# Kernel tuning notes

Measured on AMD Instinct MI355X. Metric: run time of the kernel, lower is better.

Reference implementation:

```python
import jax, jax.numpy as jnp
import numpy as np

N, E = 50000, 800000
IN_DIM, HID, H1, H2, NCLS = 512, 64, 4, 1, 40
NEG_SLOPE = 0.2


def gat_conv(x, src, dst, W, att_src, att_dst, b, heads, ch):
    # x: [N, F_in]; W: [F_in, heads*ch]; att_*: [heads, ch]; b: [heads*ch]
    n = x.shape[0]
    h = (x @ W).reshape(n, heads, ch)                      # [N,H,C]
    a_s = jnp.einsum('nhc,hc->nh', h, att_src)             # [N,H]
    a_d = jnp.einsum('nhc,hc->nh', h, att_dst)             # [N,H]
    e = jax.nn.leaky_relu(a_s[src] + a_d[dst], NEG_SLOPE)  # [E,H]
    # segment softmax over incoming edges of each destination node
    m = jax.ops.segment_max(e, dst, num_segments=n)        # [N,H]
    ex = jnp.exp(e - m[dst])
    s = jax.ops.segment_sum(ex, dst, num_segments=n)       # [N,H]
    alpha = ex / (s[dst] + 1e-16)                          # [E,H]
    out = jax.ops.segment_sum(alpha[:, :, None] * h[src], dst, num_segments=n)
    return out.reshape(n, heads * ch) + b


def setup_inputs() -> dict:
    key = jax.random.key(0)
    ks = jax.random.split(key, 10)
    glorot = lambda k, shp: jax.random.normal(k, shp, jnp.float32) * jnp.sqrt(2.0 / (shp[0] + shp[-1]))
    return {
        'x': jax.random.normal(ks[0], (N, IN_DIM), jnp.float32),
        'edge_index': jax.random.randint(ks[1], (2, E), 0, N, jnp.int64),
        'W1': glorot(ks[2], (IN_DIM, H1 * HID)),
        'att_src1': glorot(ks[3], (H1, HID)),
        'att_dst1': glorot(ks[4], (H1, HID)),
        'b1': jnp.zeros((H1 * HID,), jnp.float32),
        'W2': glorot(ks[5], (H1 * HID, H2 * NCLS)),
        'att_src2': glorot(ks[6], (H2, NCLS)),
        'att_dst2': glorot(ks[7], (H2, NCLS)),
        'b2': jnp.zeros((H2 * NCLS,), jnp.float32),
    }


def reference(x, edge_index, W1, att_src1, att_dst1, b1, W2, att_src2, att_dst2, b2):
    n = x.shape[0]
    loops = jnp.arange(n, dtype=edge_index.dtype)
    src = jnp.concatenate([edge_index[0], loops])  # add self loops (PyG default)
    dst = jnp.concatenate([edge_index[1], loops])
    # dropout layers are identity in eval mode
    h = gat_conv(x, src, dst, W1, att_src1, att_dst1, b1, H1, HID)
    h = jax.nn.elu(h)
    out = gat_conv(h, src, dst, W2, att_src2, att_dst2, b2, H2, NCLS)
    return jax.nn.log_softmax(out, axis=1)
```

## Files before the change

kernel.cpp:

```cpp
#include <hip/hip_runtime.h>
#include <math.h>
#include <stdint.h>


typedef short bf16x8 __attribute__((ext_vector_type(8)));
typedef float f32x4  __attribute__((ext_vector_type(4)));

static __device__ __forceinline__ float leaky(float x){ return x > 0.f ? x : 0.2f*x; }
static __device__ __forceinline__ unsigned short f2bf(float f){
  uint32_t u = __float_as_uint(f);
  uint32_t r = u + 0x7fffu + ((u >> 16) & 1u);
  return (unsigned short)(r >> 16);
}
static __device__ __forceinline__ float bf2f(unsigned short u){
  return __uint_as_float(((uint32_t)u) << 16);
}

__global__ void k_cvt_x(const float* __restrict__ x, unsigned short* __restrict__ xb, int n4){
  int i = blockIdx.x*blockDim.x + threadIdx.x;
  if (i >= n4) return;
  float4 v = ((const float4*)x)[i];
  ushort4 o; o.x=f2bf(v.x); o.y=f2bf(v.y); o.z=f2bf(v.z); o.w=f2bf(v.w);
  ((ushort4*)xb)[i] = o;
}

__global__ void k_cvt_w(const float* __restrict__ W, unsigned short* __restrict__ wt){
  int i = blockIdx.x*blockDim.x + threadIdx.x;
  if (i >= 512*256) return;
  int k = i >> 8, n = i & 255;
  wt[n*512 + k] = f2bf(W[i]);
}

__global__ void k_count(const int* __restrict__ ei, int E, int n, int* __restrict__ deg){
  int i = blockIdx.x*blockDim.x + threadIdx.x;
  int tot = E + n;
  if (i >= tot) return;
  int dst = (i < E) ? ei[E + i] : (i - E);
  atomicAdd(&deg[dst], 1);
}

__global__ __launch_bounds__(256) void k_scan_a(const int* __restrict__ deg,
    int* __restrict__ rowstart, int* __restrict__ bsum, int n){
  __shared__ int sm[256];
  int b = blockIdx.x, t = threadIdx.x;
  int i = b*256 + t;
  int v = (i < n) ? deg[i] : 0;
  sm[t] = v;
  __syncthreads();
  for (int off=1; off<256; off<<=1){
    int u = (t >= off) ? sm[t-off] : 0;
    __syncthreads();
    sm[t] += u;
    __syncthreads();
  }
  if (i < n) rowstart[i+1] = sm[t];
  if (t == 255) bsum[b] = sm[255];
}
__global__ __launch_bounds__(256) void k_scan_b(int* __restrict__ bsum, int nb){
  __shared__ int sm[256];
  int t = threadIdx.x;
  int v = (t < nb) ? bsum[t] : 0;
  sm[t] = v;
  __syncthreads();
  for (int off=1; off<256; off<<=1){
    int u = (t >= off) ? sm[t-off] : 0;
    __syncthreads();
    sm[t] += u;
    __syncthreads();
  }
  if (t < nb) bsum[t] = sm[t] - v;
}
__global__ __launch_bounds__(256) void k_scan_c(int* __restrict__ rowstart,
    const int* __restrict__ bsum, int n){
  int b = blockIdx.x, t = threadIdx.x;
  int i = b*256 + t;
  if (i < n) rowstart[i+1] += bsum[b];
  if (i == 0) rowstart[0] = 0;
}

__global__ void k_fill(const int* __restrict__ ei, int E, int n,
                       const int* __restrict__ rowstart, int* __restrict__ cur, int* __restrict__ csr){
  int i = blockIdx.x*blockDim.x + threadIdx.x;
  int tot = E + n;
  if (i >= tot) return;
  int src, dst;
  if (i < E){ src = ei[i]; dst = ei[E+i]; } else { src = i - E; dst = src; }
  int pos = atomicAdd(&cur[dst], 1);
  csr[rowstart[dst] + pos] = src;
}

__global__ __launch_bounds__(256) void k_gemm1_mfma(const unsigned short* __restrict__ A,
                                                    const unsigned short* __restrict__ BT,
                                                    unsigned short* __restrict__ Cb, int M){
  __shared__ __align__(16) unsigned short lA[4*128*8];
  __shared__ __align__(16) unsigned short lB[4*128*8];
  const int t = threadIdx.x;
  const int lane = t & 63, w = t >> 6;
  const int wx = w & 1, wy = w >> 1;
  const int row0 = blockIdx.x * 128, col0 = blockIdx.y * 128;

  f32x4 acc[4][4];
  #pragma unroll
  for (int i=0;i<4;i++)
    #pragma unroll
    for (int j=0;j<4;j++)
      #pragma unroll
      for (int r=0;r<4;r++) acc[i][j][r] = 0.f;

  const int c0 = t, c1 = t + 256;
  const int r0 = c0 & 127, kq0 = c0 >> 7;
  const int r1 = c1 & 127, kq1 = c1 >> 7;
  const size_t gA0 = (size_t)min(row0 + r0, M-1)*512 + kq0*8;
  const size_t gA1 = (size_t)min(row0 + r1, M-1)*512 + kq1*8;
  const size_t gB0 = (size_t)(col0 + r0)*512 + kq0*8;
  const size_t gB1 = (size_t)(col0 + r1)*512 + kq1*8;

  const int kq = lane >> 4, li = lane & 15;

  for (int kt = 0; kt < 512; kt += 32){
    __builtin_amdgcn_global_load_lds((const __attribute__((address_space(1))) void*)(A + gA0 + kt),
        (__attribute__((address_space(3))) void*)&lA[c0*8], 16, 0, 0);
    __builtin_amdgcn_global_load_lds((const __attribute__((address_space(1))) void*)(A + gA1 + kt),
        (__attribute__((address_space(3))) void*)&lA[c1*8], 16, 0, 0);
    __builtin_amdgcn_global_load_lds((const __attribute__((address_space(1))) void*)(BT + gB0 + kt),
        (__attribute__((address_space(3))) void*)&lB[c0*8], 16, 0, 0);
    __builtin_amdgcn_global_load_lds((const __attribute__((address_space(1))) void*)(BT + gB1 + kt),
        (__attribute__((address_space(3))) void*)&lB[c1*8], 16, 0, 0);
    __syncthreads();

    bf16x8 af[4], bfr[4];
    #pragma unroll
    for (int i=0;i<4;i++){
      af[i]  = *(const bf16x8*)&lA[(kq*128 + wx*64 + i*16 + li)*8];
      bfr[i] = *(const bf16x8*)&lB[(kq*128 + wy*64 + i*16 + li)*8];
    }
    #pragma unroll
    for (int i=0;i<4;i++)
      #pragma unroll
      for (int j=0;j<4;j++)
        acc[i][j] = __builtin_amdgcn_mfma_f32_16x16x32_bf16(af[i], bfr[j], acc[i][j], 0, 0, 0);
    __syncthreads();
  }

  #pragma unroll
  for (int i=0;i<4;i++){
    #pragma unroll
    for (int r=0;r<4;r++){
      int row = row0 + wx*64 + i*16 + kq*4 + r;
      if (row < M){
        #pragma unroll
        for (int j=0;j<4;j++)
          Cb[(size_t)row*256 + col0 + wy*64 + j*16 + li] = f2bf(acc[i][j][r]);
      }
    }
  }
}

__global__ __launch_bounds__(256) void k_att1(const unsigned short* __restrict__ h1b,
    const float* __restrict__ sw, const float* __restrict__ dw,
    float* __restrict__ as1, float* __restrict__ ad1, int n){
  int lane = threadIdx.x & 63;
  int node = blockIdx.x*4 + (threadIdx.x >> 6);
  if (node >= n) return;
  ushort4 hu = *(const ushort4*)(h1b + (size_t)node*256 + lane*4);
  float hx=bf2f(hu.x), hy=bf2f(hu.y), hz=bf2f(hu.z), hw=bf2f(hu.w);
  float4 sv = *(const float4*)(sw + lane*4);
  float4 dv = *(const float4*)(dw + lane*4);
  float ps = hx*sv.x + hy*sv.y + hz*sv.z + hw*sv.w;
  float pd = hx*dv.x + hy*dv.y + hz*dv.z + hw*dv.w;
  #pragma unroll
  for (int o=1;o<16;o<<=1){ ps += __shfl_xor(ps,o); pd += __shfl_xor(pd,o); }
  if ((lane & 15) == 0){
    int h = lane >> 4;
    as1[node*4+h] = ps;
    ad1[node*4+h] = pd;
  }
}

__global__ __launch_bounds__(256) void k_agg1(const unsigned short* __restrict__ h1b,
    const float* __restrict__ as1, const float* __restrict__ ad1,
    const int* __restrict__ rowstart, const int* __restrict__ csr,
    const float* __restrict__ b1, unsigned short* __restrict__ hactb, int n){
  int lane = threadIdx.x & 63;
  int node = blockIdx.x*4 + (threadIdx.x >> 6);
  if (node >= n) return;
  int lo = rowstart[node], hi = rowstart[node+1];
  float4 adv = *(const float4*)(ad1 + node*4);
  float m0=-INFINITY, m1=-INFINITY, m2=-INFINITY, m3=-INFINITY;
  for (int e = lo + lane; e < hi; e += 64){
    int s = csr[e];
    float4 asv = *(const float4*)(as1 + s*4);
    m0 = fmaxf(m0, leaky(asv.x + adv.x));
    m1 = fmaxf(m1, leaky(asv.y + adv.y));
    m2 = fmaxf(m2, leaky(asv.z + adv.z));
    m3 = fmaxf(m3, leaky(asv.w + adv.w));
  }
  #pragma unroll
  for (int o=1;o<64;o<<=1){
    m0 = fmaxf(m0, __shfl_xor(m0,o));
    m1 = fmaxf(m1, __shfl_xor(m1,o));
    m2 = fmaxf(m2, __shfl_xor(m2,o));
    m3 = fmaxf(m3, __shfl_xor(m3,o));
  }
  int h = lane >> 4;
  float mh  = (h==0)?m0:(h==1)?m1:(h==2)?m2:m3;
  float adh = (h==0)?adv.x:(h==1)?adv.y:(h==2)?adv.z:adv.w;
  float ax=0.f, ay=0.f, az=0.f, aw=0.f, ssum=0.f;
  int e = lo;
  for (; e + 3 < hi; e += 4){
    int s0 = csr[e], s1 = csr[e+1], s2 = csr[e+2], s3 = csr[e+3];
    float x0 = __expf(leaky(as1[s0*4+h] + adh) - mh);
    float x1 = __expf(leaky(as1[s1*4+h] + adh) - mh);
    float x2 = __expf(leaky(as1[s2*4+h] + adh) - mh);
    float x3 = __expf(leaky(as1[s3*4+h] + adh) - mh);
    ushort4 u0 = *(const ushort4*)(h1b + (size_t)s0*256 + lane*4);
    ushort4 u1 = *(const ushort4*)(h1b + (size_t)s1*256 + lane*4);
    ushort4 u2 = *(const ushort4*)(h1b + (size_t)s2*256 + lane*4);
    ushort4 u3 = *(const ushort4*)(h1b + (size_t)s3*256 + lane*4);
    ax += x0*bf2f(u0.x) + x1*bf2f(u1.x) + x2*bf2f(u2.x) + x3*bf2f(u3.x);
    ay += x0*bf2f(u0.y) + x1*bf2f(u1.y) + x2*bf2f(u2.y) + x3*bf2f(u3.y);
    az += x0*bf2f(u0.z) + x1*bf2f(u1.z) + x2*bf2f(u2.z) + x3*bf2f(u3.z);
    aw += x0*bf2f(u0.w) + x1*bf2f(u1.w) + x2*bf2f(u2.w) + x3*bf2f(u3.w);
    ssum += x0 + x1 + x2 + x3;
  }
  for (; e < hi; ++e){
    int s0 = csr[e];
    float x0 = __expf(leaky(as1[s0*4+h] + adh) - mh);
    ushort4 u0 = *(const ushort4*)(h1b + (size_t)s0*256 + lane*4);
    ax += x0*bf2f(u0.x); ay += x0*bf2f(u0.y); az += x0*bf2f(u0.z); aw += x0*bf2f(u0.w);
    ssum += x0;
  }
  float inv = 1.f/(ssum + 1e-16f);
  float4 bv = *(const float4*)(b1 + lane*4);
  float o0 = ax*inv + bv.x, o1 = ay*inv + bv.y, o2 = az*inv + bv.z, o3 = aw*inv + bv.w;
  ushort4 r;
  r.x = f2bf(o0 > 0.f ? o0 : expm1f(o0));
  r.y = f2bf(o1 > 0.f ? o1 : expm1f(o1));
  r.z = f2bf(o2 > 0.f ? o2 : expm1f(o2));
  r.w = f2bf(o3 > 0.f ? o3 : expm1f(o3));
  *(ushort4*)(hactb + (size_t)node*256 + lane*4) = r;
}

__global__ __launch_bounds__(256) void k_gemm2(const unsigned short* __restrict__ A,
    const float* __restrict__ B, const float* __restrict__ sw, const float* __restrict__ dw,
    unsigned short* __restrict__ Cb, float* __restrict__ as2, float* __restrict__ ad2, int M){
  __shared__ float Xl[32][129];
  __shared__ float Wl[128*40];
  __shared__ float Sps[32][8], Spd[32][8];
  int t = threadIdx.x;
  int row0 = blockIdx.x*32;
  int r = t & 31, g = t >> 5;
  float acc[5] = {0,0,0,0,0};
  for (int kt=0; kt<256; kt+=128){
    for (int i=t; i<1280; i+=256)
      *(float4*)&Wl[i*4] = *(const float4*)(B + kt*40 + i*4);
    for (int i=t; i<512; i+=256){
      int rr = i >> 4, k8 = i & 15;
      int grow = row0 + rr; if (grow >= M) grow = M-1;
      uint4 v = *(const uint4*)(A + (size_t)grow*256 + kt + k8*8);
      float* xp = &Xl[rr][k8*8];
      xp[0] = __uint_as_float(v.x << 16); xp[1] = __uint_as_float(v.x & 0xffff0000u);
      xp[2] = __uint_as_float(v.y << 16); xp[3] = __uint_as_float(v.y & 0xffff0000u);
      xp[4] = __uint_as_float(v.z << 16); xp[5] = __uint_as_float(v.z & 0xffff0000u);
      xp[6] = __uint_as_float(v.w << 16); xp[7] = __uint_as_float(v.w & 0xffff0000u);
    }
    __syncthreads();
    #pragma unroll 4
    for (int k=0;k<128;++k){
      float a = Xl[r][k];
      const float* wp = &Wl[k*40 + g*5];
      #pragma unroll
      for (int j=0;j<5;++j) acc[j] += a * wp[j];
    }
    __syncthreads();
  }
  int grow = row0 + r;
  float ps = 0.f, pd = 0.f;
  #pragma unroll
  for (int j=0;j<5;++j){
    ps += acc[j] * sw[g*5+j];
    pd += acc[j] * dw[g*5+j];
  }
  Sps[r][g] = ps; Spd[r][g] = pd;
  if (grow < M){
    #pragma unroll
    for (int j=0;j<5;++j) Cb[(size_t)grow*40 + g*5 + j] = f2bf(acc[j]);
  }
  __syncthreads();
  if (t < 32){
    float a = 0.f, b = 0.f;
    #pragma unroll
    for (int g2=0; g2<8; ++g2){ a += Sps[t][g2]; b += Spd[t][g2]; }
    int rw = row0 + t;
    if (rw < M){ as2[rw] = a; ad2[rw] = b; }
  }
}

__global__ __launch_bounds__(256) void k_agg2(const unsigned short* __restrict__ h2b,
    const float* __restrict__ as2, const float* __restrict__ ad2,
    const int* __restrict__ rowstart, const int* __restrict__ csr,
    const float* __restrict__ b2, float* __restrict__ out, int n){
  int lane = threadIdx.x & 63;
  int node = blockIdx.x*4 + (threadIdx.x >> 6);
  if (node >= n) return;
  int lo = rowstart[node], hi = rowstart[node+1];
  int deg = hi - lo;
  float adn = ad2[node];
  int   sl = 0;
  float ll = -INFINITY;
  if (lane < deg){ sl = csr[lo + lane]; ll = leaky(as2[sl] + adn); }
  float m = ll;
  for (int e = lo + lane + 64; e < hi; e += 64)
    m = fmaxf(m, leaky(as2[csr[e]] + adn));
  #pragma unroll
  for (int o=1;o<64;o<<=1) m = fmaxf(m, __shfl_xor(m,o));

  bool act = lane < 40;
  float acc = 0.f, psum = 0.f;
  for (int c = lo; c < hi; c += 64){
    int cnt = min(64, hi - c);
    int   s_l; float ex_l;
    if (c == lo){
      s_l = sl; ex_l = (lane < cnt) ? __expf(ll - m) : 0.f;
    } else {
      s_l = 0; ex_l = 0.f;
      if (lane < cnt){ s_l = csr[c + lane]; ex_l = __expf(leaky(as2[s_l] + adn) - m); }
    }
    psum += ex_l;
    int j = 0;
    for (; j + 3 < cnt; j += 4){
      int   s0=__shfl(s_l,j),  s1=__shfl(s_l,j+1),  s2=__shfl(s_l,j+2),  s3=__shfl(s_l,j+3);
      float e0=__shfl(ex_l,j), e1=__shfl(ex_l,j+1), e2=__shfl(ex_l,j+2), e3=__shfl(ex_l,j+3);
      float h0 = act ? bf2f(h2b[(size_t)s0*40 + lane]) : 0.f;
      float h1 = act ? bf2f(h2b[(size_t)s1*40 + lane]) : 0.f;
      float h2 = act ? bf2f(h2b[(size_t)s2*40 + lane]) : 0.f;
      float h3 = act ? bf2f(h2b[(size_t)s3*40 + lane]) : 0.f;
      acc += e0*h0; acc += e1*h1; acc += e2*h2; acc += e3*h3;
    }
    for (; j < cnt; ++j){
      int s0=__shfl(s_l,j); float e0=__shfl(ex_l,j);
      acc += e0 * (act ? bf2f(h2b[(size_t)s0*40 + lane]) : 0.f);
    }
  }
  float ssum = psum;
  #pragma unroll
  for (int o=1;o<64;o<<=1) ssum += __shfl_xor(ssum,o);
  float ov = acc/(ssum + 1e-16f) + (act ? b2[lane] : 0.f);
  float v = act ? ov : -INFINITY;
  float mx = v;
  #pragma unroll
  for (int o=1;o<64;o<<=1) mx = fmaxf(mx, __shfl_xor(mx,o));
  float ev = act ? __expf(ov - mx) : 0.f;
  float se = ev;
  #pragma unroll
  for (int o=1;o<64;o<<=1) se += __shfl_xor(se,o);
  if (act) out[(size_t)node*40 + lane] = (ov - mx) - __logf(se);
}

extern "C" void kernel_launch(void* const* d_in, const int* in_sizes, int n_in,
                              void* d_out, int out_size, void* d_ws, size_t ws_size,
                              hipStream_t stream){
  const float* x   = (const float*)d_in[0];
  const int*   ei  = (const int*)d_in[1];
  const float* W1  = (const float*)d_in[2];
  const float* s1w = (const float*)d_in[3];
  const float* d1w = (const float*)d_in[4];
  const float* b1  = (const float*)d_in[5];
  const float* W2  = (const float*)d_in[6];
  const float* s2w = (const float*)d_in[7];
  const float* d2w = (const float*)d_in[8];
  const float* b2  = (const float*)d_in[9];
  float* out = (float*)d_out;

  const int N  = in_sizes[0] / 512;
  const int E  = in_sizes[1] / 2;
  const int Et = E + N;

  float* f = (float*)d_ws;
  unsigned short* h1b   = (unsigned short*)f;  f += (size_t)N*128;
  unsigned short* hactb = (unsigned short*)f;  f += (size_t)N*128;
  float* as1  = f;  f += (size_t)N*4;
  float* ad1  = f;  f += (size_t)N*4;
  float* as2  = f;  f += N;
  float* ad2  = f;  f += N;
  unsigned short* w1t = (unsigned short*)f;  f += 256*512/2;
  unsigned short* xb  = (unsigned short*)f;  f += (size_t)N*256;
  unsigned short* h2b = xb;
  int* ip = (int*)f;
  int* rowstart = ip;  ip += (N + 4) & ~3;
  int* deg      = ip;  ip += N;
  int* cur      = ip;  ip += N;
  int* csr      = ip;  ip += Et;
  int* bsum     = ip;  ip += 256;

  int nb4 = (N + 3) / 4;
  int n4  = (N*512)/4;
  int nbs = (N + 255) / 256;
  k_cvt_x<<<(n4+255)/256, 256, 0, stream>>>(x, xb, n4);
  k_cvt_w<<<512, 256, 0, stream>>>(W1, w1t);
  hipMemsetAsync(deg, 0, (size_t)2*N*sizeof(int), stream);
  k_count<<<(Et+255)/256, 256, 0, stream>>>(ei, E, N, deg);
  k_scan_a<<<nbs, 256, 0, stream>>>(deg, rowstart, bsum, N);
  k_scan_b<<<1, 256, 0, stream>>>(bsum, nbs);
  k_scan_c<<<nbs, 256, 0, stream>>>(rowstart, bsum, N);
  k_fill <<<(Et+255)/256, 256, 0, stream>>>(ei, E, N, rowstart, cur, csr);
  k_gemm1_mfma<<<dim3((N+127)/128, 2), 256, 0, stream>>>(xb, w1t, h1b, N);
  k_att1 <<<nb4, 256, 0, stream>>>(h1b, s1w, d1w, as1, ad1, N);
  k_agg1 <<<nb4, 256, 0, stream>>>(h1b, as1, ad1, rowstart, csr, b1, hactb, N);
  k_gemm2<<<(N+31)/32, 256, 0, stream>>>(hactb, W2, s2w, d2w, h2b, as2, ad2, N);
  k_agg2 <<<nb4, 256, 0, stream>>>(h2b, as2, ad2, rowstart, csr, b2, out, N);
}
```

Baseline: 488.2 us.

## Fuse attention logits into GEMM1 epilogue and share edge weights across lanes in agg1

The attention-score kernel k_att1 is removed. Its dot products with att_src/att_dst are now computed in the MFMA GEMM epilogue from fp32 accumulators, which saves a full reread of h1 and one launch. In k_agg1, each lane now computes the softmax weight for one (edge, head) pair, 16 edges per chunk. Source indices and exp weights are then broadcast with shuffles instead of every lane recomputing them, which cuts the redundant as1 loads and exp calls per edge. The trade-off is extra shuffle traffic and more epilogue work in the GEMM, and the logits now come from unrounded fp32 accumulators rather than bf16 values.

```diff
diff --git a/kernel.cpp b/kernel.cpp
--- a/kernel.cpp
+++ b/kernel.cpp
@@ -91,7 +91,11 @@
 
 __global__ __launch_bounds__(256) void k_gemm1_mfma(const unsigned short* __restrict__ A,
                                                     const unsigned short* __restrict__ BT,
-                                                    unsigned short* __restrict__ Cb, int M){
+                                                    const float* __restrict__ SW,
+                                                    const float* __restrict__ DW,
+                                                    unsigned short* __restrict__ Cb,
+                                                    float* __restrict__ as1,
+                                                    float* __restrict__ ad1, int M){
   __shared__ __align__(16) unsigned short lA[4*128*8];
   __shared__ __align__(16) unsigned short lB[4*128*8];
   const int t = threadIdx.x;
@@ -154,26 +158,28 @@
       }
     }
   }
-}
-
-__global__ __launch_bounds__(256) void k_att1(const unsigned short* __restrict__ h1b,
-    const float* __restrict__ sw, const float* __restrict__ dw,
-    float* __restrict__ as1, float* __restrict__ ad1, int n){
-  int lane = threadIdx.x & 63;
-  int node = blockIdx.x*4 + (threadIdx.x >> 6);
-  if (node >= n) return;
-  ushort4 hu = *(const ushort4*)(h1b + (size_t)node*256 + lane*4);
-  float hx=bf2f(hu.x), hy=bf2f(hu.y), hz=bf2f(hu.z), hw=bf2f(hu.w);
-  float4 sv = *(const float4*)(sw + lane*4);
-  float4 dv = *(const float4*)(dw + lane*4);
-  float ps = hx*sv.x + hy*sv.y + hz*sv.z + hw*sv.w;
-  float pd = hx*dv.x + hy*dv.y + hz*dv.z + hw*dv.w;
-  #pragma unroll
-  for (int o=1;o<16;o<<=1){ ps += __shfl_xor(ps,o); pd += __shfl_xor(pd,o); }
-  if ((lane & 15) == 0){
-    int h = lane >> 4;
-    as1[node*4+h] = ps;
-    ad1[node*4+h] = pd;
+
+  const int hw = (int)blockIdx.y*2 + wy;
+  float sv[4], dv[4];
+  #pragma unroll
+  for (int j=0;j<4;j++){
+    sv[j] = SW[hw*64 + j*16 + li];
+    dv[j] = DW[hw*64 + j*16 + li];
+  }
+  #pragma unroll
+  for (int i=0;i<4;i++){
+    #pragma unroll
+    for (int r=0;r<4;r++){
+      float ps = acc[i][0][r]*sv[0] + acc[i][1][r]*sv[1] + acc[i][2][r]*sv[2] + acc[i][3][r]*sv[3];
+      float pd = acc[i][0][r]*dv[0] + acc[i][1][r]*dv[1] + acc[i][2][r]*dv[2] + acc[i][3][r]*dv[3];
+      #pragma unroll
+      for (int o=1;o<16;o<<=1){ ps += __shfl_xor(ps,o); pd += __shfl_xor(pd,o); }
+      int row = row0 + wx*64 + i*16 + kq*4 + r;
+      if (li == 0 && row < M){
+        as1[row*4 + hw] = ps;
+        ad1[row*4 + hw] = pd;
+      }
+    }
   }
 }
 
@@ -185,51 +191,52 @@
   int node = blockIdx.x*4 + (threadIdx.x >> 6);
   if (node >= n) return;
   int lo = rowstart[node], hi = rowstart[node+1];
-  float4 adv = *(const float4*)(ad1 + node*4);
-  float m0=-INFINITY, m1=-INFINITY, m2=-INFINITY, m3=-INFINITY;
-  for (int e = lo + lane; e < hi; e += 64){
-    int s = csr[e];
-    float4 asv = *(const float4*)(as1 + s*4);
-    m0 = fmaxf(m0, leaky(asv.x + adv.x));
-    m1 = fmaxf(m1, leaky(asv.y + adv.y));
-    m2 = fmaxf(m2, leaky(asv.z + adv.z));
-    m3 = fmaxf(m3, leaky(asv.w + adv.w));
-  }
-  #pragma unroll
-  for (int o=1;o<64;o<<=1){
-    m0 = fmaxf(m0, __shfl_xor(m0,o));
-    m1 = fmaxf(m1, __shfl_xor(m1,o));
-    m2 = fmaxf(m2, __shfl_xor(m2,o));
-    m3 = fmaxf(m3, __shfl_xor(m3,o));
-  }
+  int jj = lane >> 2, hh = lane & 3;
+  float adh_p = ad1[node*4 + hh];
+
+  float m = -INFINITY;
+  for (int c = lo + jj; c < hi; c += 16){
+    int s = csr[c];
+    m = fmaxf(m, leaky(as1[s*4 + hh] + adh_p));
+  }
+  #pragma unroll
+  for (int o=4;o<64;o<<=1) m = fmaxf(m, __shfl_xor(m,o));
+
   int h = lane >> 4;
-  float mh  = (h==0)?m0:(h==1)?m1:(h==2)?m2:m3;
-  float adh = (h==0)?adv.x:(h==1)?adv.y:(h==2)?adv.z:adv.w;
-  float ax=0.f, ay=0.f, az=0.f, aw=0.f, ssum=0.f;
-  int e = lo;
-  for (; e + 3 < hi; e += 4){
-    int s0 = csr[e], s1 = csr[e+1], s2 = csr[e+2], s3 = csr[e+3];
-    float x0 = __expf(leaky(as1[s0*4+h] + adh) - mh);
-    float x1 = __expf(leaky(as1[s1*4+h] + adh) - mh);
-    float x2 = __expf(leaky(as1[s2*4+h] + adh) - mh);
-    float x3 = __expf(leaky(as1[s3*4+h] + adh) - mh);
-    ushort4 u0 = *(const ushort4*)(h1b + (size_t)s0*256 + lane*4);
-    ushort4 u1 = *(const ushort4*)(h1b + (size_t)s1*256 + lane*4);
-    ushort4 u2 = *(const ushort4*)(h1b + (size_t)s2*256 + lane*4);
-    ushort4 u3 = *(const ushort4*)(h1b + (size_t)s3*256 + lane*4);
-    ax += x0*bf2f(u0.x) + x1*bf2f(u1.x) + x2*bf2f(u2.x) + x3*bf2f(u3.x);
-    ay += x0*bf2f(u0.y) + x1*bf2f(u1.y) + x2*bf2f(u2.y) + x3*bf2f(u3.y);
-    az += x0*bf2f(u0.z) + x1*bf2f(u1.z) + x2*bf2f(u2.z) + x3*bf2f(u3.z);
-    aw += x0*bf2f(u0.w) + x1*bf2f(u1.w) + x2*bf2f(u2.w) + x3*bf2f(u3.w);
-    ssum += x0 + x1 + x2 + x3;
-  }
-  for (; e < hi; ++e){
-    int s0 = csr[e];
-    float x0 = __expf(leaky(as1[s0*4+h] + adh) - mh);
-    ushort4 u0 = *(const ushort4*)(h1b + (size_t)s0*256 + lane*4);
-    ax += x0*bf2f(u0.x); ay += x0*bf2f(u0.y); az += x0*bf2f(u0.z); aw += x0*bf2f(u0.w);
-    ssum += x0;
-  }
+  float ax=0.f, ay=0.f, az=0.f, aw=0.f, psum=0.f;
+  for (int c = lo; c < hi; c += 16){
+    int cnt = min(16, hi - c);
+    int s_l = 0; float ex_l = 0.f;
+    if (jj < cnt){
+      s_l = csr[c + jj];
+      ex_l = __expf(leaky(as1[s_l*4 + hh] + adh_p) - m);
+    }
+    psum += ex_l;
+    int j = 0;
+    for (; j + 3 < cnt; j += 4){
+      int   s0 = __shfl(s_l, j*4),      s1 = __shfl(s_l, j*4+4),
+            s2 = __shfl(s_l, j*4+8),    s3 = __shfl(s_l, j*4+12);
+      float e0 = __shfl(ex_l, j*4+h),   e1 = __shfl(ex_l, j*4+4+h),
+            e2 = __shfl(ex_l, j*4+8+h), e3 = __shfl(ex_l, j*4+12+h);
+      ushort4 u0 = *(const ushort4*)(h1b + (size_t)s0*256 + lane*4);
+      ushort4 u1 = *(const ushort4*)(h1b + (size_t)s1*256 + lane*4);
+      ushort4 u2 = *(const ushort4*)(h1b + (size_t)s2*256 + lane*4);
+      ushort4 u3 = *(const ushort4*)(h1b + (size_t)s3*256 + lane*4);
+      ax += e0*bf2f(u0.x) + e1*bf2f(u1.x) + e2*bf2f(u2.x) + e3*bf2f(u3.x);
+      ay += e0*bf2f(u0.y) + e1*bf2f(u1.y) + e2*bf2f(u2.y) + e3*bf2f(u3.y);
+      az += e0*bf2f(u0.z) + e1*bf2f(u1.z) + e2*bf2f(u2.z) + e3*bf2f(u3.z);
+      aw += e0*bf2f(u0.w) + e1*bf2f(u1.w) + e2*bf2f(u2.w) + e3*bf2f(u3.w);
+    }
+    for (; j < cnt; ++j){
+      int   s0 = __shfl(s_l, j*4);
+      float e0 = __shfl(ex_l, j*4+h);
+      ushort4 u0 = *(const ushort4*)(h1b + (size_t)s0*256 + lane*4);
+      ax += e0*bf2f(u0.x); ay += e0*bf2f(u0.y); az += e0*bf2f(u0.z); aw += e0*bf2f(u0.w);
+    }
+  }
+  #pragma unroll
+  for (int o=4;o<64;o<<=1) psum += __shfl_xor(psum,o);
+  float ssum = __shfl(psum, h);
   float inv = 1.f/(ssum + 1e-16f);
   float4 bv = *(const float4*)(b1 + lane*4);
   float o0 = ax*inv + bv.x, o1 = ay*inv + bv.y, o2 = az*inv + bv.z, o3 = aw*inv + bv.w;
@@ -404,8 +411,7 @@
   k_scan_b<<<1, 256, 0, stream>>>(bsum, nbs);
   k_scan_c<<<nbs, 256, 0, stream>>>(rowstart, bsum, N);
   k_fill <<<(Et+255)/256, 256, 0, stream>>>(ei, E, N, rowstart, cur, csr);
-  k_gemm1_mfma<<<dim3((N+127)/128, 2), 256, 0, stream>>>(xb, w1t, h1b, N);
-  k_att1 <<<nb4, 256, 0, stream>>>(h1b, s1w, d1w, as1, ad1, N);
+  k_gemm1_mfma<<<dim3((N+127)/128, 2), 256, 0, stream>>>(xb, w1t, s1w, d1w, h1b, as1, ad1, N);
   k_agg1 <<<nb4, 256, 0, stream>>>(h1b, as1, ad1, rowstart, csr, b1, hactb, N);
   k_gemm2<<<(N+31)/32, 256, 0, stream>>>(hactb, W2, s2w, d2w, h2b, as2, ad2, N);
   k_agg2 <<<nb4, 256, 0, stream>>>(h2b, as2, ad2, rowstart, csr, b2, out, N);
```

Result: faster. 474.2 us (-2.9%).
